# Optimization experiments

Hardware: AMD Instinct MI355X
Metric: run time of the kernel (lower is better)

The kernel has to match this reference:

```python
import jax, jax.numpy as jnp
import numpy as np

DIM = 128

def setup_inputs() -> dict:
    key = jax.random.key(0)
    ks = jax.random.split(key, 4)
    N, C, L = 64, DIM, 4096
    scale = 1.0 / np.sqrt(DIM)
    return {
        "x": jax.random.normal(ks[0], (N, C, L), dtype=jnp.float32),
        "Wq": jax.random.normal(ks[1], (DIM, DIM), dtype=jnp.float32) * scale,
        "bq": jnp.zeros((DIM,), dtype=jnp.float32),
        "Wk": jax.random.normal(ks[2], (DIM, DIM), dtype=jnp.float32) * scale,
        "bk": jnp.zeros((DIM,), dtype=jnp.float32),
        "Wv": jax.random.normal(ks[3], (DIM, DIM), dtype=jnp.float32) * scale,
        "bv": jnp.zeros((DIM,), dtype=jnp.float32),
    }

def reference(x, Wq, bq, Wk, bk, Wv, bv):
    # x: [N, C, L] -> rearrange to [N, L, C]
    h = jnp.transpose(x, (0, 2, 1))                       # [N, L, C]
    q = jnp.einsum('nlc,cd->nld', h, Wq) + bq             # [N, L, D]
    k = jnp.einsum('nlc,cd->nld', h, Wk) + bk             # [N, L, D]
    v = jnp.einsum('nlc,cd->nld', h, Wv) + bv             # [N, L, D]
    # AFT-Simple: softmax over sequence axis of K, global weighted pool of V
    w = jax.nn.softmax(k, axis=1)                         # [N, L, D]
    pooled = jnp.sum(w * v, axis=1, keepdims=True)        # [N, 1, D]
    out = jax.nn.sigmoid(q) * pooled                      # [N, L, D]
    return jnp.transpose(out, (0, 2, 1))                  # [N, C, L]
```

## Files before the change

kernel.cpp:

```cpp
#include <hip/hip_runtime.h>
#include <hip/hip_bf16.h>

#define NB 64
#define CD 128
#define LL 4096
#define LCHUNK 64
#define NCHUNK 64
#define NBG 8
#define CPB 8

typedef __attribute__((ext_vector_type(8))) short short8;
typedef __attribute__((ext_vector_type(4))) float f32x4;
typedef __attribute__((ext_vector_type(16))) float f32x16;
typedef __attribute__((ext_vector_type(2))) unsigned u32x2;
typedef __attribute__((ext_vector_type(4))) unsigned u32x4;

#define LOG2E 1.4426950408889634f

#define WT_OFF   0
#define WSS_OFF  (1u<<20)
#define WSP_OFF  ((1u<<20) + NB*NBG*CD*4)
#define POOL_OFF ((1u<<20) + 2u*NB*NBG*CD*4)
#define WSQ_OFF  (8u<<20)

__device__ __forceinline__ unsigned short f2bf(float f) {
    union { float f; unsigned u; } v; v.f = f;
    unsigned r = v.u + 0x7FFFu + ((v.u >> 16) & 1u);
    return (unsigned short)(r >> 16);
}
__device__ __forceinline__ float bf2f(unsigned short h) {
    union { unsigned u; float f; } v; v.u = ((unsigned)h) << 16;
    return v.f;
}
__device__ __forceinline__ unsigned pack2(float lo, float hi) {
    union { __hip_bfloat162 h; unsigned u; } v;
    v.h = __float22bfloat162_rn(float2{lo, hi});
    return v.u;
}
__device__ __forceinline__ f32x4 gload16f(const float* p) {
    f32x4 d;
    asm volatile("global_load_dwordx4 %0, %1, off"
                 : "=&v"(d) : "v"((unsigned long long)(uintptr_t)p));
    return d;
}

__global__ void prep_wt(const float* __restrict__ Wq, const float* __restrict__ Wk,
                        const float* __restrict__ Wv, unsigned short* __restrict__ wt) {
    int t = blockIdx.x >> 7;
    int d = blockIdx.x & 127;
    const float* W = (t == 0) ? Wq : (t == 1) ? Wk : Wv;
    int c = threadIdx.x;
    wt[((size_t)t*CD + d)*CD + c] = f2bf(W[c*CD + d]);
}

__device__ __forceinline__ void stage_x_write(char* bufx, int f, int cp, f32x4 lo, f32x4 hi) {
    char* base = bufx + (4*f)*272 + 16*((cp >> 2) ^ (f & 7)) + 4*(cp & 3);
#pragma unroll
    for (int j = 0; j < 4; ++j)
        *(unsigned*)(base + j*272) = pack2(lo[j], hi[j]);
}

__global__ __launch_bounds__(512)
void aft_qkv(const float* __restrict__ x, const unsigned short* __restrict__ wt,
             const float* __restrict__ bq, const float* __restrict__ bk,
             const float* __restrict__ bv,
             float* __restrict__ wsS, float* __restrict__ wsP,
             unsigned short* __restrict__ wsq) {
    __shared__ char lds_w[98304];
    __shared__ char lds_x[2][17408];
    __shared__ float red_s[4][32];
    __shared__ float red_p[4][32];
    const int tid = threadIdx.x;
    const int n = blockIdx.x >> 3;
    const int bg = blockIdx.x & 7;
    const int ww = tid >> 6, lane = tid & 63;
    const int u = lane & 31, h = lane >> 5;
    const int lh = ww & 1, ng = ww >> 1;
    const int d = 32*ng + u;
    const int f = tid & 15, tg = tid >> 4;

#pragma unroll
    for (int k = 0; k < 12; ++k) {
        int bi = tid + 512*k;
        u32x4 v = *(const u32x4*)((const char*)wt + (size_t)bi*16);
        *(u32x4*)(lds_w + 256*(bi >> 4) + 16*((bi & 15) ^ ((bi >> 4) & 7))) = v;
    }
    {
        const int l0 = bg*CPB*LCHUNK;
#pragma unroll
        for (int it = 0; it < 2; ++it) {
            int cp = tg + 32*it;
            f32x4 lo = *(const f32x4*)(x + ((size_t)n*CD + 2*cp    )*LL + l0 + 4*f);
            f32x4 hi = *(const f32x4*)(x + ((size_t)n*CD + 2*cp + 1)*LL + l0 + 4*f);
            stage_x_write(lds_x[0], f, cp, lo, hi);
        }
    }
    const float bql = bq[d], bkl = bk[d], bvl = bv[d];
    float s_run = 0.f, p_run = 0.f;
    __syncthreads();

#pragma unroll 1
    for (int t = 0; t < CPB; ++t) {
        const int l0 = (bg*CPB + t) * LCHUNK;
        f32x4 pf0, pf1, pf2, pf3;
        if (t + 1 < CPB) {
            const float* xb = x + (size_t)n*CD*LL + (l0 + LCHUNK) + 4*f;
            pf0 = gload16f(xb + (size_t)(2*tg     )*LL);
            pf1 = gload16f(xb + (size_t)(2*tg + 1 )*LL);
            pf2 = gload16f(xb + (size_t)(2*(tg+32)    )*LL);
            pf3 = gload16f(xb + (size_t)(2*(tg+32) + 1)*LL);
        }
        const char* abase = lds_x[t & 1] + 272*(32*lh + u);
        const int asw = ((32*lh + u) >> 2) & 7;
        const char* wb = lds_w + 256*d;
        const int dsw = d & 7;
        f32x16 aq = {0,0,0,0,0,0,0,0,0,0,0,0,0,0,0,0};
        f32x16 ak = {0,0,0,0,0,0,0,0,0,0,0,0,0,0,0,0};
        f32x16 av = {0,0,0,0,0,0,0,0,0,0,0,0,0,0,0,0};
#pragma unroll
        for (int kk = 0; kk < 8; ++kk) {
            const int cb = 2*kk + h;
            short8 a   = *(const short8*)(abase + 16*(cb ^ asw));
            short8 wqf = *(const short8*)(wb           + 16*(cb ^ dsw));
            short8 wkf = *(const short8*)(wb + 32768   + 16*(cb ^ dsw));
            short8 wvf = *(const short8*)(wb + 65536   + 16*(cb ^ dsw));
            aq = __builtin_amdgcn_mfma_f32_32x32x16_bf16(a, wqf, aq, 0,0,0);
            ak = __builtin_amdgcn_mfma_f32_32x32x16_bf16(a, wkf, ak, 0,0,0);
            av = __builtin_amdgcn_mfma_f32_32x32x16_bf16(a, wvf, av, 0,0,0);
        }
#pragma unroll
        for (int grp = 0; grp < 4; ++grp) {
            float sg[4];
#pragma unroll
            for (int e = 0; e < 4; ++e) {
                const int reg = 4*grp + e;
                float ex = __builtin_amdgcn_exp2f((ak[reg] + bkl) * LOG2E);
                s_run += ex;
                p_run += ex * (av[reg] + bvl);
                float q2 = (aq[reg] + bql) * LOG2E;
                sg[e] = __builtin_amdgcn_rcpf(1.f + __builtin_amdgcn_exp2f(-q2));
            }
            u32x2 val = { pack2(sg[0], sg[1]), pack2(sg[2], sg[3]) };
            *(u32x2*)(wsq + ((size_t)n*CD + d)*LL + l0 + 32*lh + 8*grp + 4*h) = val;
        }
        if (t + 1 < CPB) {
            asm volatile("s_waitcnt vmcnt(0)" ::: "memory");
            __builtin_amdgcn_sched_barrier(0);
            char* nb = lds_x[(t + 1) & 1];
            stage_x_write(nb, f, tg,      pf0, pf1);
            stage_x_write(nb, f, tg + 32, pf2, pf3);
        }
        __syncthreads();
    }

    s_run += __shfl_xor(s_run, 32, 64);
    p_run += __shfl_xor(p_run, 32, 64);
    if (lh == 1 && h == 0) { red_s[ng][u] = s_run; red_p[ng][u] = p_run; }
    __syncthreads();
    if (lh == 0 && h == 0) {
        size_t idx = ((size_t)n*NBG + bg)*CD + d;
        wsS[idx] = s_run + red_s[ng][u];
        wsP[idx] = p_run + red_p[ng][u];
    }
}

__global__ void aft_pass2(const float* __restrict__ wsS, const float* __restrict__ wsP,
                          float* __restrict__ pooled) {
    int n = blockIdx.x, d = threadIdx.x;
    float s = 0.f, p = 0.f;
    for (int b = 0; b < NBG; ++b) {
        size_t idx = ((size_t)n*NBG + b)*CD + d;
        s += wsS[idx];
        p += wsP[idx];
    }
    pooled[(size_t)n*CD + d] = p / s;
}

__global__ __launch_bounds__(256)
void aft_pass3(const unsigned short* __restrict__ wsq, const float* __restrict__ pooled,
               float* __restrict__ out) {
    const int b = blockIdx.x;
    const int n = b >> 8;
    const int d = (b >> 1) & 127;
    const int half = b & 1;
    const float pl = pooled[(size_t)n*CD + d];
    const size_t base = ((size_t)n*CD + d)*LL + half*2048 + threadIdx.x*8;
    short8 v = *(const short8*)(wsq + base);
    f32x4 o0, o1;
#pragma unroll
    for (int j = 0; j < 4; ++j) {
        o0[j] = bf2f((unsigned short)v[j]) * pl;
        o1[j] = bf2f((unsigned short)v[4+j]) * pl;
    }
    *(f32x4*)(out + base) = o0;
    *(f32x4*)(out + base + 4) = o1;
}

extern "C" void kernel_launch(void* const* d_in, const int* in_sizes, int n_in,
                              void* d_out, int out_size, void* d_ws, size_t ws_size,
                              hipStream_t stream) {
    const float* x  = (const float*)d_in[0];
    const float* Wq = (const float*)d_in[1];
    const float* bq = (const float*)d_in[2];
    const float* Wk = (const float*)d_in[3];
    const float* bk = (const float*)d_in[4];
    const float* Wv = (const float*)d_in[5];
    const float* bv = (const float*)d_in[6];
    float* out = (float*)d_out;
    char* ws = (char*)d_ws;
    unsigned short* wt = (unsigned short*)(ws + WT_OFF);
    float* wsS = (float*)(ws + WSS_OFF);
    float* wsP = (float*)(ws + WSP_OFF);
    float* pooled = (float*)(ws + POOL_OFF);
    unsigned short* wsq = (unsigned short*)(ws + WSQ_OFF);

    prep_wt<<<384, 128, 0, stream>>>(Wq, Wk, Wv, wt);
    aft_qkv<<<NB * NBG, 512, 0, stream>>>(x, wt, bq, bk, bv, wsS, wsP, wsq);
    aft_pass2<<<NB, CD, 0, stream>>>(wsS, wsP, pooled);
    aft_pass3<<<NB * CD * 2, 256, 0, stream>>>(wsq, pooled, out);
}
```

Measured before the change: 102.5 us.

## Give each wave two 32-row L tiles to reuse weight fragments across MFMAs

Each wave now computes two 32-row L tiles per iteration, so every weight fragment read from LDS feeds six MFMAs instead of three. Each iteration handles a 128-wide L chunk, which halves the loop count and doubles the prefetch to eight global loads. The two x-staging buffers are now filled together, so the earlier ping-pong double buffering becomes a single-stage scheme guarded by two barriers per iteration. A waves_per_eu(2,2) hint is added to give the extra accumulators room, at the cost of less overlap between LDS staging and compute.

```diff
diff --git a/kernel.cpp b/kernel.cpp
--- a/kernel.cpp
+++ b/kernel.cpp
@@ -4,10 +4,9 @@
 #define NB 64
 #define CD 128
 #define LL 4096
-#define LCHUNK 64
 #define NCHUNK 64
 #define NBG 8
-#define CPB 8
+#define NIT 4
 
 typedef __attribute__((ext_vector_type(8))) short short8;
 typedef __attribute__((ext_vector_type(4))) float f32x4;
@@ -60,14 +59,14 @@
         *(unsigned*)(base + j*272) = pack2(lo[j], hi[j]);
 }
 
-__global__ __launch_bounds__(512)
+__global__ __launch_bounds__(512) __attribute__((amdgpu_waves_per_eu(2, 2)))
 void aft_qkv(const float* __restrict__ x, const unsigned short* __restrict__ wt,
              const float* __restrict__ bq, const float* __restrict__ bk,
              const float* __restrict__ bv,
              float* __restrict__ wsS, float* __restrict__ wsP,
              unsigned short* __restrict__ wsq) {
     __shared__ char lds_w[98304];
-    __shared__ char lds_x[2][17408];
+    __shared__ char lds_x[2 * 17408];
     __shared__ float red_s[4][32];
     __shared__ float red_p[4][32];
     const int tid = threadIdx.x;
@@ -75,9 +74,11 @@
     const int bg = blockIdx.x & 7;
     const int ww = tid >> 6, lane = tid & 63;
     const int u = lane & 31, h = lane >> 5;
-    const int lh = ww & 1, ng = ww >> 1;
+    const int ch2 = ww >> 2, ng = ww & 3;
     const int d = 32*ng + u;
     const int f = tid & 15, tg = tid >> 4;
+    const int lbase = bg * (NIT * 128);
+    const size_t xb0 = (size_t)n*CD*LL;
 
 #pragma unroll
     for (int k = 0; k < 12; ++k) {
@@ -85,79 +86,101 @@
         u32x4 v = *(const u32x4*)((const char*)wt + (size_t)bi*16);
         *(u32x4*)(lds_w + 256*(bi >> 4) + 16*((bi & 15) ^ ((bi >> 4) & 7))) = v;
     }
-    {
-        const int l0 = bg*CPB*LCHUNK;
-#pragma unroll
-        for (int it = 0; it < 2; ++it) {
-            int cp = tg + 32*it;
-            f32x4 lo = *(const f32x4*)(x + ((size_t)n*CD + 2*cp    )*LL + l0 + 4*f);
-            f32x4 hi = *(const f32x4*)(x + ((size_t)n*CD + 2*cp + 1)*LL + l0 + 4*f);
-            stage_x_write(lds_x[0], f, cp, lo, hi);
-        }
-    }
+#pragma unroll
+    for (int c2 = 0; c2 < 2; ++c2)
+#pragma unroll
+        for (int itg = 0; itg < 2; ++itg) {
+            int cp = tg + 32*itg;
+            const float* p = x + xb0 + (size_t)(2*cp)*LL + lbase + 64*c2 + 4*f;
+            f32x4 lo = *(const f32x4*)p;
+            f32x4 hi = *(const f32x4*)(p + LL);
+            stage_x_write(lds_x + c2*17408, f, cp, lo, hi);
+        }
     const float bql = bq[d], bkl = bk[d], bvl = bv[d];
     float s_run = 0.f, p_run = 0.f;
     __syncthreads();
 
+    const char* ax = lds_x + ch2*17408;
+    const char* wbq = lds_w + 256*d;
+    const int dsw = d & 7;
+
 #pragma unroll 1
-    for (int t = 0; t < CPB; ++t) {
-        const int l0 = (bg*CPB + t) * LCHUNK;
-        f32x4 pf0, pf1, pf2, pf3;
-        if (t + 1 < CPB) {
-            const float* xb = x + (size_t)n*CD*LL + (l0 + LCHUNK) + 4*f;
-            pf0 = gload16f(xb + (size_t)(2*tg     )*LL);
-            pf1 = gload16f(xb + (size_t)(2*tg + 1 )*LL);
-            pf2 = gload16f(xb + (size_t)(2*(tg+32)    )*LL);
-            pf3 = gload16f(xb + (size_t)(2*(tg+32) + 1)*LL);
-        }
-        const char* abase = lds_x[t & 1] + 272*(32*lh + u);
-        const int asw = ((32*lh + u) >> 2) & 7;
-        const char* wb = lds_w + 256*d;
-        const int dsw = d & 7;
-        f32x16 aq = {0,0,0,0,0,0,0,0,0,0,0,0,0,0,0,0};
-        f32x16 ak = {0,0,0,0,0,0,0,0,0,0,0,0,0,0,0,0};
-        f32x16 av = {0,0,0,0,0,0,0,0,0,0,0,0,0,0,0,0};
+    for (int it = 0; it < NIT; ++it) {
+        const int l0 = lbase + it*128;
+        f32x4 pf0, pf1, pf2, pf3, pf4, pf5, pf6, pf7;
+        if (it + 1 < NIT) {
+            const float* pb = x + xb0 + l0 + 128 + 4*f;
+            pf0 = gload16f(pb + (size_t)(2*tg     )*LL);
+            pf1 = gload16f(pb + (size_t)(2*tg + 1 )*LL);
+            pf2 = gload16f(pb + (size_t)(2*(tg+32)    )*LL);
+            pf3 = gload16f(pb + (size_t)(2*(tg+32) + 1)*LL);
+            pf4 = gload16f(pb + (size_t)(2*tg     )*LL + 64);
+            pf5 = gload16f(pb + (size_t)(2*tg + 1 )*LL + 64);
+            pf6 = gload16f(pb + (size_t)(2*(tg+32)    )*LL + 64);
+            pf7 = gload16f(pb + (size_t)(2*(tg+32) + 1)*LL + 64);
+        }
+        f32x16 aq[2], ak[2], av[2];
+#pragma unroll
+        for (int lt = 0; lt < 2; ++lt) {
+            aq[lt] = (f32x16){0,0,0,0,0,0,0,0,0,0,0,0,0,0,0,0};
+            ak[lt] = (f32x16){0,0,0,0,0,0,0,0,0,0,0,0,0,0,0,0};
+            av[lt] = (f32x16){0,0,0,0,0,0,0,0,0,0,0,0,0,0,0,0};
+        }
 #pragma unroll
         for (int kk = 0; kk < 8; ++kk) {
             const int cb = 2*kk + h;
-            short8 a   = *(const short8*)(abase + 16*(cb ^ asw));
-            short8 wqf = *(const short8*)(wb           + 16*(cb ^ dsw));
-            short8 wkf = *(const short8*)(wb + 32768   + 16*(cb ^ dsw));
-            short8 wvf = *(const short8*)(wb + 65536   + 16*(cb ^ dsw));
-            aq = __builtin_amdgcn_mfma_f32_32x32x16_bf16(a, wqf, aq, 0,0,0);
-            ak = __builtin_amdgcn_mfma_f32_32x32x16_bf16(a, wkf, ak, 0,0,0);
-            av = __builtin_amdgcn_mfma_f32_32x32x16_bf16(a, wvf, av, 0,0,0);
-        }
-#pragma unroll
-        for (int grp = 0; grp < 4; ++grp) {
-            float sg[4];
-#pragma unroll
-            for (int e = 0; e < 4; ++e) {
-                const int reg = 4*grp + e;
-                float ex = __builtin_amdgcn_exp2f((ak[reg] + bkl) * LOG2E);
-                s_run += ex;
-                p_run += ex * (av[reg] + bvl);
-                float q2 = (aq[reg] + bql) * LOG2E;
-                sg[e] = __builtin_amdgcn_rcpf(1.f + __builtin_amdgcn_exp2f(-q2));
+            short8 a0  = *(const short8*)(ax + 272*(u     ) + 16*(cb ^ ((u >> 2) & 7)));
+            short8 a1  = *(const short8*)(ax + 272*(u + 32) + 16*(cb ^ ((u >> 2) & 7)));
+            short8 wqf = *(const short8*)(wbq           + 16*(cb ^ dsw));
+            short8 wkf = *(const short8*)(wbq + 32768   + 16*(cb ^ dsw));
+            short8 wvf = *(const short8*)(wbq + 65536   + 16*(cb ^ dsw));
+            aq[0] = __builtin_amdgcn_mfma_f32_32x32x16_bf16(a0, wqf, aq[0], 0,0,0);
+            ak[0] = __builtin_amdgcn_mfma_f32_32x32x16_bf16(a0, wkf, ak[0], 0,0,0);
+            av[0] = __builtin_amdgcn_mfma_f32_32x32x16_bf16(a0, wvf, av[0], 0,0,0);
+            aq[1] = __builtin_amdgcn_mfma_f32_32x32x16_bf16(a1, wqf, aq[1], 0,0,0);
+            ak[1] = __builtin_amdgcn_mfma_f32_32x32x16_bf16(a1, wkf, ak[1], 0,0,0);
+            av[1] = __builtin_amdgcn_mfma_f32_32x32x16_bf16(a1, wvf, av[1], 0,0,0);
+        }
+#pragma unroll
+        for (int lt = 0; lt < 2; ++lt) {
+#pragma unroll
+            for (int grp = 0; grp < 4; ++grp) {
+                float sg[4];
+#pragma unroll
+                for (int e = 0; e < 4; ++e) {
+                    const int reg = 4*grp + e;
+                    float ex = __builtin_amdgcn_exp2f((ak[lt][reg] + bkl) * LOG2E);
+                    s_run += ex;
+                    p_run += ex * (av[lt][reg] + bvl);
+                    float q2 = (aq[lt][reg] + bql) * LOG2E;
+                    sg[e] = __builtin_amdgcn_rcpf(1.f + __builtin_amdgcn_exp2f(-q2));
+                }
+                u32x2 val = { pack2(sg[0], sg[1]), pack2(sg[2], sg[3]) };
+                *(u32x2*)(wsq + ((size_t)n*CD + d)*LL
+                          + l0 + 64*ch2 + 32*lt + 8*grp + 4*h) = val;
             }
-            u32x2 val = { pack2(sg[0], sg[1]), pack2(sg[2], sg[3]) };
-            *(u32x2*)(wsq + ((size_t)n*CD + d)*LL + l0 + 32*lh + 8*grp + 4*h) = val;
-        }
-        if (t + 1 < CPB) {
-            asm volatile("s_waitcnt vmcnt(0)" ::: "memory");
-            __builtin_amdgcn_sched_barrier(0);
-            char* nb = lds_x[(t + 1) & 1];
-            stage_x_write(nb, f, tg,      pf0, pf1);
-            stage_x_write(nb, f, tg + 32, pf2, pf3);
-        }
-        __syncthreads();
+        }
+        if (it + 1 < NIT) {
+            asm volatile("s_waitcnt vmcnt(8)" ::: "memory");
+            __builtin_amdgcn_sched_barrier(0);
+            __builtin_amdgcn_s_barrier();
+            __builtin_amdgcn_sched_barrier(0);
+            stage_x_write(lds_x,         f, tg,      pf0, pf1);
+            stage_x_write(lds_x,         f, tg + 32, pf2, pf3);
+            stage_x_write(lds_x + 17408, f, tg,      pf4, pf5);
+            stage_x_write(lds_x + 17408, f, tg + 32, pf6, pf7);
+            asm volatile("s_waitcnt lgkmcnt(0)" ::: "memory");
+            __builtin_amdgcn_sched_barrier(0);
+            __builtin_amdgcn_s_barrier();
+            __builtin_amdgcn_sched_barrier(0);
+        }
     }
 
     s_run += __shfl_xor(s_run, 32, 64);
     p_run += __shfl_xor(p_run, 32, 64);
-    if (lh == 1 && h == 0) { red_s[ng][u] = s_run; red_p[ng][u] = p_run; }
+    if (ch2 == 1 && h == 0) { red_s[ng][u] = s_run; red_p[ng][u] = p_run; }
     __syncthreads();
-    if (lh == 0 && h == 0) {
+    if (ch2 == 0 && h == 0) {
         size_t idx = ((size_t)n*NBG + bg)*CD + d;
         wsS[idx] = s_run + red_s[ng][u];
         wsP[idx] = p_run + red_p[ng][u];
```

Measured after the change: 110.1 us. +7.4%, slower.
